# Kernel tuning notes

Hardware: AMD Instinct MI355X
Metric: run time of the kernel (lower is better)

Reference implementation:

```python
import jax, jax.numpy as jnp
import numpy as np

N = 100000      # total nodes across all graphs
E = 1600000     # total directed edges (pred -> node)
F = 128         # feat_size
H = 128         # hidden_size
M = 128         # message_size
G = 8           # number of graphs in batch
NP = N // G     # nodes per graph (num_nodes entries, all equal)
CRITIC_W = 0.5  # critic_agg_weight


def _lin_init(key, fan_in, fan_out):
    s = 1.0 / np.sqrt(fan_in)
    return jax.random.uniform(key, (fan_in, fan_out), jnp.float32, -s, s)


def setup_inputs() -> dict:
    key = jax.random.key(0)
    ks = jax.random.split(key, 20)
    inputs = jax.random.normal(ks[0], (N, F), jnp.float32)
    edge_src = jax.random.randint(ks[1], (E,), 0, N)
    edge_dst = jax.random.randint(ks[2], (E,), 0, N)
    actions = jax.random.randint(ks[3], (G,), 0, NP)
    return {
        'inputs': inputs,
        'W_in': _lin_init(ks[4], F, H), 'b_in': jnp.zeros((H,), jnp.float32),
        'W_msg': _lin_init(ks[5], H, M), 'b_msg': jnp.zeros((M,), jnp.float32),
        'W_upd': _lin_init(ks[6], M + H, H), 'b_upd': jnp.zeros((H,), jnp.float32),
        'W_a1': _lin_init(ks[7], H, 16), 'b_a1': jnp.zeros((16,), jnp.float32),
        'W_a2': _lin_init(ks[8], 16, 1), 'b_a2': jnp.zeros((1,), jnp.float32),
        'W_c1': _lin_init(ks[9], H, 16), 'b_c1': jnp.zeros((16,), jnp.float32),
        'W_c2': _lin_init(ks[10], 16, 1), 'b_c2': jnp.zeros((1,), jnp.float32),
        'edge_src': edge_src, 'edge_dst': edge_dst, 'actions': actions,
    }


def reference(inputs, W_in, b_in, W_msg, b_msg, W_upd, b_upd,
              W_a1, b_a1, W_a2, b_a2, W_c1, b_c1, W_c2, b_c2,
              edge_src, edge_dst, actions):
    # InputModel: Linear + ReLU  (send_input=True)
    node_states = jax.nn.relu(inputs @ W_in + b_in)          # [N, H]
    # MessageModel: Linear + ReLU
    messages = jax.nn.relu(node_states @ W_msg + b_msg)      # [N, M]
    # _aggregate_all: per-node sum over predecessor messages (segment-sum over edges)
    agg = jax.ops.segment_sum(messages[edge_src], edge_dst, num_segments=N)  # [N, M]
    # UpdateModel: Linear(M+H, H) + ReLU (no goal)
    updates = jax.nn.relu(jnp.concatenate([agg, node_states], axis=1) @ W_upd + b_upd)  # [N, H]
    # ActorModel: per-node logit
    logits_all = (jax.nn.relu(updates @ W_a1 + b_a1) @ W_a2 + b_a2).reshape(G, NP)
    # CriticModel: per-node score, per-graph weighted max/mean pooling
    crit_all = (jax.nn.relu(updates @ W_c1 + b_c1) @ W_c2 + b_c2).reshape(G, NP)
    v = (crit_all.max(axis=1) * CRITIC_W + crit_all.mean(axis=1) * (1.0 - CRITIC_W))[:, None]  # [G,1]
    # Categorical(logits) per graph: log_prob of given action + entropy
    logp = jax.nn.log_softmax(logits_all, axis=1)            # [G, NP]
    log_prob = jnp.take_along_axis(logp, actions[:, None], axis=1)  # [G,1]
    ent = -jnp.sum(jnp.exp(logp) * logp, axis=1, keepdims=True)     # [G,1]
    return updates, actions, log_prob, ent, v
```

## Files before the change

### kernel.cpp

```cpp
#include <hip/hip_runtime.h>
#include <math.h>

typedef unsigned short u16;
typedef unsigned int   u32;
typedef unsigned char  u8;
typedef __attribute__((ext_vector_type(8))) short short8v;
typedef __attribute__((ext_vector_type(4))) float f32x4;
typedef __attribute__((ext_vector_type(2))) float f32x2;

__device__ __forceinline__ u16 f2bf(float x) {
    u32 u = __float_as_uint(x);
    u += 0x7FFFu + ((u >> 16) & 1u);
    return (u16)(u >> 16);
}

#if __has_builtin(__builtin_amdgcn_cvt_pk_fp8_f32) && __has_builtin(__builtin_amdgcn_cvt_pk_f32_fp8)
#define HW_FP8 1
#endif

__device__ __forceinline__ u8 f2fp8(float v) {
#ifdef HW_FP8
    return (u8)(__builtin_amdgcn_cvt_pk_fp8_f32(v, v, 0, false) & 0xFF);
#else
    if (v < 0.015625f) return (u8)__float2int_rn(v * 512.0f);
    u32 b = __float_as_uint(fminf(v, 448.0f));
    b += 0x7FFFF + ((b >> 20) & 1);
    return (u8)((((b >> 23) - 120) << 3) | ((b >> 20) & 7));
#endif
}

__device__ __forceinline__ void fp8x4_acc(u32 w, float* acc) {
#ifdef HW_FP8
    const f32x2 lo = __builtin_amdgcn_cvt_pk_f32_fp8(w, false);
    const f32x2 hi = __builtin_amdgcn_cvt_pk_f32_fp8(w, true);
    acc[0] += lo[0]; acc[1] += lo[1]; acc[2] += hi[0]; acc[3] += hi[1];
#else
#pragma unroll
    for (int i = 0; i < 4; ++i) {
        const u32 b = (w >> (8 * i)) & 0xFF;
        const u32 e = (b >> 3) & 15, m = b & 7;
        acc[i] += e ? __uint_as_float(((e + 120) << 23) | (m << 20))
                    : (float)m * 0x1p-9f;
    }
#endif
}

#define NPB        256
#define NPB_SHIFT  8
#define EBUF_CAP   4608
#define MAX_BUK    512
#define BCS        16
#define BIN_CHUNK  4096

__global__ __launch_bounds__(256) void conv_kernel(
    const float* __restrict__ W_in, const float* __restrict__ W_msg,
    const float* __restrict__ W_upd,
    const float* __restrict__ Wa1, const float* __restrict__ Wc1,
    u16* __restrict__ Wt_in, u16* __restrict__ Wt_msg,
    u16* __restrict__ Wt_upd, u16* __restrict__ Wh,
    int* __restrict__ bcursor)
{
    const int idx = blockIdx.x * 256 + threadIdx.x;
    if (idx < 16384) {
        const int c = idx >> 7, k = idx & 127;
        Wt_in[c * 128 + k] = f2bf(W_in[k * 128 + c]);
    } else if (idx < 32768) {
        const int i = idx - 16384;
        const int c = i >> 7, k = i & 127;
        Wt_msg[c * 128 + k] = f2bf(W_msg[k * 128 + c]);
    } else if (idx < 65536) {
        const int i = idx - 32768;
        const int c = i >> 8, k = i & 255;
        Wt_upd[c * 256 + k] = f2bf(W_upd[k * 128 + c]);
    } else if (idx < 69632) {
        const int i = idx - 65536;
        const int col = i >> 7, k = i & 127;
        const float v = (col < 16) ? Wa1[k * 16 + col] : Wc1[k * 16 + (col - 16)];
        Wh[col * 128 + k] = f2bf(v);
    } else if (idx < 69632 + MAX_BUK * BCS) {
        bcursor[idx - 69632] = 0;
    }
}

__global__ __launch_bounds__(1024) void bin_gemm1_kernel(
    const int* __restrict__ src, const int* __restrict__ dst,
    int* __restrict__ bcursor, int* __restrict__ ebuf,
    int E, int nbuk, int binGrid, int g1Grid,
    const float* __restrict__ X, const u16* __restrict__ Wt_in,
    const float* __restrict__ b_in, u16* __restrict__ ns, int rows)
{
    __shared__ u16 smem[128 * 136];
    const int tid = threadIdx.x;

    const int mn   = min(binGrid, g1Grid);
    const int half = 2 * mn;
    int role, widx;
    if ((int)blockIdx.x < half) {
        role = (int)blockIdx.x & 1;
        widx = (int)blockIdx.x >> 1;
    } else {
        const int r = (int)blockIdx.x - half;
        role = (binGrid > g1Grid) ? 1 : 0;
        widx = mn + r;
    }

    if (role == 1) {
        int* lcount = (int*)smem;
        int* lbase  = lcount + MAX_BUK;
        const int e0 = widx * BIN_CHUNK;
        const int e1 = min(e0 + BIN_CHUNK, E);
        for (int b = tid; b < nbuk; b += 1024) lcount[b] = 0;
        __syncthreads();

        int pay[4];
        u32 brk[4];
#pragma unroll
        for (int k = 0; k < 4; ++k) {
            const int i = e0 + tid + k * 1024;
            int payv = 0; u32 brkv = 0xFFFFFFFFu;
            if (i < e1) {
                const int d = dst[i];
                const int b = d >> NPB_SHIFT;
                const int r = atomicAdd(&lcount[b], 1);
                payv = (src[i] << NPB_SHIFT) | (d & (NPB - 1));
                brkv = ((u32)b << 16) | (u32)r;
            }
            pay[k] = payv; brk[k] = brkv;
        }
        __syncthreads();

        for (int b = tid; b < nbuk; b += 1024) {
            const int c = lcount[b];
            lbase[b] = c ? atomicAdd(&bcursor[b * BCS], c) : 0;
        }
        __syncthreads();

#pragma unroll
        for (int k = 0; k < 4; ++k) {
            if (brk[k] != 0xFFFFFFFFu) {
                const int b = (int)(brk[k] >> 16);
                const int p = lbase[b] + (int)(brk[k] & 0xFFFFu);
                ebuf[b * EBUF_CAP + min(p, EBUF_CAP - 1)] = pay[k];
            }
        }
        return;
    }

    u16 (*WtL)[136] = (u16(*)[136])smem;
    for (int i = tid; i < 2048; i += 1024)
        *(uint4*)&WtL[i >> 4][(i & 15) * 8] = ((const uint4*)Wt_in)[i];

    const int lane = tid & 63, wave = tid >> 6;
    const int lrow = lane & 15, lk = lane >> 4;
    const int r0 = widx * 256 + wave * 16;
    const int arow = r0 + lrow;
    const bool rowok = arow < rows;

    short8v a[4];
#pragma unroll
    for (int ks = 0; ks < 4; ++ks) {
        const int k = ks * 32 + lk * 8;
        short8v av = {};
        if (rowok) {
            const float* pf = X + (size_t)arow * 128 + k;
            const float4 x0 = *(const float4*)pf;
            const float4 x1 = *(const float4*)(pf + 4);
            u16 t[8] = {f2bf(x0.x), f2bf(x0.y), f2bf(x0.z), f2bf(x0.w),
                        f2bf(x1.x), f2bf(x1.y), f2bf(x1.z), f2bf(x1.w)};
            av = *(short8v*)t;
        }
        a[ks] = av;
    }
    __syncthreads();

    f32x4 acc[8];
#pragma unroll
    for (int n = 0; n < 8; ++n) acc[n] = (f32x4){0.f, 0.f, 0.f, 0.f};
#pragma unroll
    for (int ks = 0; ks < 4; ++ks) {
#pragma unroll
        for (int n = 0; n < 8; ++n) {
            const short8v b = *(const short8v*)&WtL[n * 16 + lrow][ks * 32 + lk * 8];
            acc[n] = __builtin_amdgcn_mfma_f32_16x16x32_bf16(a[ks], b, acc[n], 0, 0, 0);
        }
    }
#pragma unroll
    for (int reg = 0; reg < 4; ++reg) {
        const int row = r0 + lk * 4 + reg;
        if (row >= rows) continue;
#pragma unroll
        for (int n = 0; n < 8; ++n) {
            const float v = fmaxf(acc[n][reg] + b_in[n * 16 + lrow], 0.f);
            ns[(size_t)row * 128 + n * 16 + lrow] = f2bf(v);
        }
    }
}

__global__ __launch_bounds__(256) void csr_gemm2_kernel(
    const int* __restrict__ ebuf, const int* __restrict__ bcursor,
    int* __restrict__ offs, int* __restrict__ csr, int N, int E, int nbuk,
    const u16* __restrict__ ns, const u16* __restrict__ Wt_msg,
    const float* __restrict__ b_msg, u8* __restrict__ msg8, int rows, int g2Grid)
{
    __shared__ u16 smem[128 * 136];
    const int tid = threadIdx.x;

    if ((int)blockIdx.x >= g2Grid) {
        int* ibuf = (int*)smem;
        int* red  = ibuf;
        int* ndeg = ibuf + 4;
        int* nofs = ibuf + 260;
        int* ws   = ibuf + 516;
        int* wp   = ibuf + 520;
        const int b = (int)blockIdx.x - g2Grid;

        int part = 0;
        for (int i = tid; i < b; i += 256) part += bcursor[i * BCS];
#pragma unroll
        for (int off = 32; off >= 1; off >>= 1) part += __shfl_xor(part, off);
        if ((tid & 63) == 0) red[tid >> 6] = part;
        __syncthreads();
        const int base = red[0] + red[1] + red[2] + red[3];

        const int cnt = min(bcursor[b * BCS], EBUF_CAP);
        const int* eb = ebuf + b * EBUF_CAP;

        ndeg[tid] = 0;
        __syncthreads();
        for (int j = tid; j < cnt; j += 256)
            atomicAdd(&ndeg[eb[j] & (NPB - 1)], 1);
        __syncthreads();

        const int lane = tid & 63, wid = tid >> 6;
        const int v = ndeg[tid];
        int x = v;
#pragma unroll
        for (int off = 1; off < 64; off <<= 1) {
            const int y = __shfl_up(x, off);
            if (lane >= off) x += y;
        }
        if (lane == 63) ws[wid] = x;
        __syncthreads();
        if (tid == 0) { int s = 0; for (int w = 0; w < 4; ++w) { wp[w] = s; s += ws[w]; } }
        __syncthreads();
        const int excl = x - v + wp[wid];
        nofs[tid] = excl;
        const int node = (b << NPB_SHIFT) + tid;
        if (node < N) offs[node] = base + excl;
        if (b == 0 && tid == 0) offs[N] = E;
        ndeg[tid] = 0;
        __syncthreads();

        for (int j = tid; j < cnt; j += 256) {
            const int e = eb[j];
            const int d = e & (NPB - 1);
            const int p = atomicAdd(&ndeg[d], 1);
            csr[base + nofs[d] + p] = e >> NPB_SHIFT;
        }
        return;
    }

    u16 (*WtL)[136] = (u16(*)[136])smem;
    for (int i = tid; i < 2048; i += 256)
        *(uint4*)&WtL[i >> 4][(i & 15) * 8] = ((const uint4*)Wt_msg)[i];

    const int lane = tid & 63, wave = tid >> 6;
    const int lrow = lane & 15, lk = lane >> 4;
    const int r0 = (int)blockIdx.x * 64 + wave * 16;
    const int arow = r0 + lrow;
    const bool rowok = arow < rows;

    short8v a[4];
#pragma unroll
    for (int ks = 0; ks < 4; ++ks) {
        short8v av = {};
        if (rowok) av = *(const short8v*)(ns + (size_t)arow * 128 + ks * 32 + lk * 8);
        a[ks] = av;
    }
    __syncthreads();

    f32x4 acc[8];
#pragma unroll
    for (int n = 0; n < 8; ++n) acc[n] = (f32x4){0.f, 0.f, 0.f, 0.f};
#pragma unroll
    for (int ks = 0; ks < 4; ++ks) {
#pragma unroll
        for (int n = 0; n < 8; ++n) {
            const short8v b = *(const short8v*)&WtL[n * 16 + lrow][ks * 32 + lk * 8];
            acc[n] = __builtin_amdgcn_mfma_f32_16x16x32_bf16(a[ks], b, acc[n], 0, 0, 0);
        }
    }
#pragma unroll
    for (int reg = 0; reg < 4; ++reg) {
        const int row = r0 + lk * 4 + reg;
        if (row >= rows) continue;
#pragma unroll
        for (int n = 0; n < 8; ++n) {
            const float v = fmaxf(acc[n][reg] + b_msg[n * 16 + lrow], 0.f);
            msg8[(size_t)row * 128 + n * 16 + lrow] = f2fp8(v);
        }
    }
}

__device__ __forceinline__ void acc16(float* acc, const uint4 u) {
    fp8x4_acc(u.x, acc);
    fp8x4_acc(u.y, acc + 4);
    fp8x4_acc(u.z, acc + 8);
    fp8x4_acc(u.w, acc + 12);
}

__global__ __launch_bounds__(256) void gather_fp8_kernel(
    const int* __restrict__ offs, const int* __restrict__ csr,
    const u8* __restrict__ msg8, u16* __restrict__ agg, int N)
{
    const int node = blockIdx.x * 32 + (threadIdx.x >> 3);
    if (node >= N) return;
    const int c16 = threadIdx.x & 7;
    int j = offs[node];
    const int j1 = offs[node + 1];
    const uint4* mv = (const uint4*)msg8;
    float acc[16];
#pragma unroll
    for (int q = 0; q < 16; ++q) acc[q] = 0.f;
    for (; j + 3 < j1; j += 4) {
        const int s0 = csr[j], s1 = csr[j + 1], s2 = csr[j + 2], s3 = csr[j + 3];
        const uint4 u0 = mv[(size_t)s0 * 8 + c16];
        const uint4 u1 = mv[(size_t)s1 * 8 + c16];
        const uint4 u2 = mv[(size_t)s2 * 8 + c16];
        const uint4 u3 = mv[(size_t)s3 * 8 + c16];
        acc16(acc, u0); acc16(acc, u1); acc16(acc, u2); acc16(acc, u3);
    }
    for (; j < j1; ++j)
        acc16(acc, mv[(size_t)csr[j] * 8 + c16]);

    u16 r[16];
#pragma unroll
    for (int q = 0; q < 16; ++q) r[q] = f2bf(acc[q]);
    uint4* ap = (uint4*)(agg + (size_t)node * 128 + c16 * 16);
    ap[0] = *(uint4*)r;
    ap[1] = *(uint4*)(r + 8);
}

__global__ __launch_bounds__(512) void gemm3_head_kernel(
    const u16* __restrict__ agg, const u16* __restrict__ ns,
    const u16* __restrict__ Wt_upd, const float* __restrict__ b_upd,
    float* __restrict__ Cf,
    const u16* __restrict__ Wh,
    const float* __restrict__ ba1, const float* __restrict__ Wa2, const float* __restrict__ ba2,
    const float* __restrict__ bc1, const float* __restrict__ Wc2, const float* __restrict__ bc2,
    float* __restrict__ logits, float* __restrict__ crit, int rows)
{
    __shared__ u16 smem[128 * 136];
    u16 (*WtL)[136] = (u16(*)[136])smem;

    const int tid = threadIdx.x;
    const uint4* W4 = (const uint4*)Wt_upd;

    for (int i = tid; i < 2048; i += 512)
        *(uint4*)&WtL[i >> 4][(i & 15) * 8] = W4[(i >> 4) * 32 + (i & 15)];

    const int lane = tid & 63, wave = tid >> 6;
    const int lrow = lane & 15, lk = lane >> 4;
    const int r0 = blockIdx.x * 128 + wave * 16;
    const int arow = r0 + lrow;
    const bool rowok = arow < rows;

    short8v a[4], a2[4];
#pragma unroll
    for (int ks = 0; ks < 4; ++ks) {
        short8v av = {}, av2 = {};
        if (rowok) {
            av  = *(const short8v*)(agg + (size_t)arow * 128 + ks * 32 + lk * 8);
            av2 = *(const short8v*)(ns  + (size_t)arow * 128 + ks * 32 + lk * 8);
        }
        a[ks] = av; a2[ks] = av2;
    }
    __syncthreads();

    f32x4 acc[8];
#pragma unroll
    for (int n = 0; n < 8; ++n) acc[n] = (f32x4){0.f, 0.f, 0.f, 0.f};
#pragma unroll
    for (int ks = 0; ks < 4; ++ks) {
#pragma unroll
        for (int n = 0; n < 8; ++n) {
            const short8v b = *(const short8v*)&WtL[n * 16 + lrow][ks * 32 + lk * 8];
            acc[n] = __builtin_amdgcn_mfma_f32_16x16x32_bf16(a[ks], b, acc[n], 0, 0, 0);
        }
    }

    __syncthreads();
    for (int i = tid; i < 2048; i += 512)
        *(uint4*)&WtL[i >> 4][(i & 15) * 8] = W4[(i >> 4) * 32 + 16 + (i & 15)];
    __syncthreads();

#pragma unroll
    for (int ks = 0; ks < 4; ++ks) {
#pragma unroll
        for (int n = 0; n < 8; ++n) {
            const short8v b = *(const short8v*)&WtL[n * 16 + lrow][ks * 32 + lk * 8];
            acc[n] = __builtin_amdgcn_mfma_f32_16x16x32_bf16(a2[ks], b, acc[n], 0, 0, 0);
        }
    }

    u16 uv[4][8];
#pragma unroll
    for (int reg = 0; reg < 4; ++reg) {
        const int row = r0 + lk * 4 + reg;
#pragma unroll
        for (int n = 0; n < 8; ++n) {
            const float v = fmaxf(acc[n][reg] + b_upd[n * 16 + lrow], 0.f);
            uv[reg][n] = f2bf(v);
            if (row < rows) Cf[(size_t)row * 128 + n * 16 + lrow] = v;
        }
    }
    __syncthreads();

    u16 (*uT)[16][136] = (u16(*)[16][136])smem;
#pragma unroll
    for (int reg = 0; reg < 4; ++reg) {
        const int lr = lk * 4 + reg;
#pragma unroll
        for (int n = 0; n < 8; ++n)
            uT[wave][lr][n * 16 + lrow] = uv[reg][n];
    }
    __syncthreads();

    short8v ah[4], b0[4], b1[4];
#pragma unroll
    for (int ks = 0; ks < 4; ++ks) {
        const int k = ks * 32 + lk * 8;
        ah[ks] = *(const short8v*)&uT[wave][lrow][k];
        b0[ks] = *(const short8v*)(Wh + (size_t)lrow * 128 + k);
        b1[ks] = *(const short8v*)(Wh + (size_t)(16 + lrow) * 128 + k);
    }
    f32x4 acc0 = (f32x4){0.f, 0.f, 0.f, 0.f};
    f32x4 acc1 = (f32x4){0.f, 0.f, 0.f, 0.f};
#pragma unroll
    for (int ks = 0; ks < 4; ++ks) {
        acc0 = __builtin_amdgcn_mfma_f32_16x16x32_bf16(ah[ks], b0[ks], acc0, 0, 0, 0);
        acc1 = __builtin_amdgcn_mfma_f32_16x16x32_bf16(ah[ks], b1[ks], acc1, 0, 0, 0);
    }
    const float wa = Wa2[lrow], wc = Wc2[lrow];
    const float ha = ba1[lrow], hc = bc1[lrow];
    const float b2a = ba2[0],   b2c = bc2[0];
#pragma unroll
    for (int reg = 0; reg < 4; ++reg) {
        float pa = fmaxf(acc0[reg] + ha, 0.f) * wa;
        float pc = fmaxf(acc1[reg] + hc, 0.f) * wc;
#pragma unroll
        for (int off = 8; off >= 1; off >>= 1) {
            pa += __shfl_xor(pa, off);
            pc += __shfl_xor(pc, off);
        }
        const int row = r0 + lk * 4 + reg;
        if (lrow == 0 && row < rows) {
            logits[row] = pa + b2a;
            crit[row]   = pc + b2c;
        }
    }
}

__device__ __forceinline__ float blockRedMax(float v, float* red) {
#pragma unroll
    for (int o = 32; o >= 1; o >>= 1) v = fmaxf(v, __shfl_xor(v, o));
    const int w = threadIdx.x >> 6;
    __syncthreads();
    if ((threadIdx.x & 63) == 0) red[w] = v;
    __syncthreads();
    if (threadIdx.x < 16) {
        float x = red[threadIdx.x];
#pragma unroll
        for (int o = 8; o >= 1; o >>= 1) x = fmaxf(x, __shfl_xor(x, o));
        if (threadIdx.x == 0) red[0] = x;
    }
    __syncthreads();
    const float r = red[0];
    __syncthreads();
    return r;
}

__device__ __forceinline__ float blockRedSum(float v, float* red) {
#pragma unroll
    for (int o = 32; o >= 1; o >>= 1) v += __shfl_xor(v, o);
    const int w = threadIdx.x >> 6;
    __syncthreads();
    if ((threadIdx.x & 63) == 0) red[w] = v;
    __syncthreads();
    if (threadIdx.x < 16) {
        float x = red[threadIdx.x];
#pragma unroll
        for (int o = 8; o >= 1; o >>= 1) x += __shfl_xor(x, o);
        if (threadIdx.x == 0) red[0] = x;
    }
    __syncthreads();
    const float r = red[0];
    __syncthreads();
    return r;
}

__global__ __launch_bounds__(1024) void finalize_kernel(
    const float* __restrict__ logits, const float* __restrict__ crit,
    const int* __restrict__ actions, float* __restrict__ out, int NP, int G)
{
    __shared__ float slog[12512];
    __shared__ float red[16];
    const int g = blockIdx.x;
    const int tid = threadIdx.x;
    const float* lg = logits + (long long)g * NP;
    const float* cg = crit   + (long long)g * NP;

    float lmax = -3.402823466e38f, cmax = -3.402823466e38f, csum = 0.f;
    for (int i = tid; i < NP; i += 1024) {
        const float l = lg[i], c = cg[i];
        slog[i] = l;
        lmax = fmaxf(lmax, l);
        cmax = fmaxf(cmax, c);
        csum += c;
    }
    __syncthreads();
    lmax = blockRedMax(lmax, red);
    cmax = blockRedMax(cmax, red);
    csum = blockRedSum(csum, red);

    float zsum = 0.f, ssum = 0.f;
    for (int i = tid; i < NP; i += 1024) {
        const float s = slog[i];
        const float e = expf(s - lmax);
        zsum += e;
        ssum += s * e;
    }
    zsum = blockRedSum(zsum, red);
    ssum = blockRedSum(ssum, red);

    if (tid == 0) {
        const int a = actions[g];
        const float sa   = slog[a];
        const float logZ = logf(zsum) + lmax;
        const float lp   = sa - logZ;
        const float H    = logZ - ssum / zsum;
        const float v    = cmax * 0.5f + (csum / (float)NP) * 0.5f;
        out[g]         = (float)a;
        out[G + g]     = lp;
        out[2 * G + g] = H;
        out[3 * G + g] = v;
    }
}

extern "C" void kernel_launch(void* const* d_in, const int* in_sizes, int n_in,
                              void* d_out, int out_size, void* d_ws, size_t ws_size,
                              hipStream_t stream)
{
    const float* inputs = (const float*)d_in[0];
    const float* W_in   = (const float*)d_in[1];
    const float* b_in   = (const float*)d_in[2];
    const float* W_msg  = (const float*)d_in[3];
    const float* b_msg  = (const float*)d_in[4];
    const float* W_upd  = (const float*)d_in[5];
    const float* b_upd  = (const float*)d_in[6];
    const float* W_a1   = (const float*)d_in[7];
    const float* b_a1   = (const float*)d_in[8];
    const float* W_a2   = (const float*)d_in[9];
    const float* b_a2   = (const float*)d_in[10];
    const float* W_c1   = (const float*)d_in[11];
    const float* b_c1   = (const float*)d_in[12];
    const float* W_c2   = (const float*)d_in[13];
    const float* b_c2   = (const float*)d_in[14];
    const int* edge_src = (const int*)d_in[15];
    const int* edge_dst = (const int*)d_in[16];
    const int* actions  = (const int*)d_in[17];

    const int N  = in_sizes[0] / 128;
    const int E  = in_sizes[15];
    const int G  = in_sizes[17];
    const int NP = N / G;
    const int nbuk = (N + NPB - 1) >> NPB_SHIFT;

    float* out = (float*)d_out;

    u16* ns_bf  = (u16*)d_ws;
    u16* agg_bf = ns_bf + (size_t)N * 128;
    u8*  msg8   = (u8*)(agg_bf + (size_t)N * 128);
    u16* Wt_in  = (u16*)(msg8 + (size_t)N * 128);
    u16* Wt_msg = Wt_in  + 128 * 128;
    u16* Wt_upd = Wt_msg + 128 * 128;
    u16* Wh     = Wt_upd + 128 * 256;
    float* logits = (float*)(Wh + 32 * 128);
    float* crit   = logits + N;
    int*   offs    = (int*)(crit + N);
    int*   csr     = offs + (N + 1);
    int*   bcursor = csr + E;
    int*   ebuf    = bcursor + MAX_BUK * BCS;

    const int binGrid = (E + BIN_CHUNK - 1) / BIN_CHUNK;
    const int convGrid = (69632 + MAX_BUK * BCS + 255) / 256;
    const int g1Grid  = (N + 255) / 256;
    const int g2Grid  = (N + 63) / 64;
    const int g3Grid  = (N + 127) / 128;

    conv_kernel<<<convGrid, 256, 0, stream>>>(
        W_in, W_msg, W_upd, W_a1, W_c1, Wt_in, Wt_msg, Wt_upd, Wh, bcursor);
    bin_gemm1_kernel<<<binGrid + g1Grid, 1024, 0, stream>>>(
        edge_src, edge_dst, bcursor, ebuf, E, nbuk, binGrid, g1Grid,
        inputs, Wt_in, b_in, ns_bf, N);
    csr_gemm2_kernel<<<g2Grid + nbuk, 256, 0, stream>>>(
        ebuf, bcursor, offs, csr, N, E, nbuk,
        ns_bf, Wt_msg, b_msg, msg8, N, g2Grid);
    gather_fp8_kernel<<<(N + 31) / 32, 256, 0, stream>>>(offs, csr, msg8, agg_bf, N);
    gemm3_head_kernel<<<g3Grid, 512, 0, stream>>>(
        agg_bf, ns_bf, Wt_upd, b_upd, out, Wh,
        b_a1, W_a2, b_a2, b_c1, W_c2, b_c2, logits, crit, N);
    finalize_kernel<<<G, 1024, 0, stream>>>(logits, crit, actions, out + (size_t)N * 128, NP, G);
}
```

Before: 145.6 us.

## Split gather and update GEMM into halves and co-schedule them in one launch

Gather and update-GEMM work is split into two row halves. The first half is gathered alone. A combined kernel then runs the GEMM+head on the first half while other blocks gather the second half, and a final launch does the GEMM for the second half. The goal is to overlap the latency-bound gather with the compute-bound MFMA GEMM and reduce tail idle time. The cost is an extra kernel launch, and gather blocks now use 512 threads while sharing a kernel with the large static LDS allocation, which could reduce occupancy.

```diff
diff --git a/kernel.cpp b/kernel.cpp
--- a/kernel.cpp
+++ b/kernel.cpp
@@ -309,13 +309,14 @@
     fp8x4_acc(u.w, acc + 12);
 }
 
-__global__ __launch_bounds__(256) void gather_fp8_kernel(
+__device__ __forceinline__ void gather_body(
+    int tid, int widx, int rowBeg, int rowEnd,
     const int* __restrict__ offs, const int* __restrict__ csr,
-    const u8* __restrict__ msg8, u16* __restrict__ agg, int N)
-{
-    const int node = blockIdx.x * 32 + (threadIdx.x >> 3);
-    if (node >= N) return;
-    const int c16 = threadIdx.x & 7;
+    const u8* __restrict__ msg8, u16* __restrict__ agg)
+{
+    const int node = rowBeg + widx * 64 + (tid >> 3);
+    if (node >= rowEnd) return;
+    const int c16 = tid & 7;
     int j = offs[node];
     const int j1 = offs[node + 1];
     const uint4* mv = (const uint4*)msg8;
@@ -341,19 +342,16 @@
     ap[1] = *(uint4*)(r + 8);
 }
 
-__global__ __launch_bounds__(512) void gemm3_head_kernel(
+__device__ __forceinline__ void gemm3_head_body(
+    u16* smem_raw, int tid, int widx, int rowBeg, int rowEnd,
     const u16* __restrict__ agg, const u16* __restrict__ ns,
     const u16* __restrict__ Wt_upd, const float* __restrict__ b_upd,
-    float* __restrict__ Cf,
-    const u16* __restrict__ Wh,
+    float* __restrict__ Cf, const u16* __restrict__ Wh,
     const float* __restrict__ ba1, const float* __restrict__ Wa2, const float* __restrict__ ba2,
     const float* __restrict__ bc1, const float* __restrict__ Wc2, const float* __restrict__ bc2,
-    float* __restrict__ logits, float* __restrict__ crit, int rows)
-{
-    __shared__ u16 smem[128 * 136];
-    u16 (*WtL)[136] = (u16(*)[136])smem;
-
-    const int tid = threadIdx.x;
+    float* __restrict__ logits, float* __restrict__ crit)
+{
+    u16 (*WtL)[136] = (u16(*)[136])smem_raw;
     const uint4* W4 = (const uint4*)Wt_upd;
 
     for (int i = tid; i < 2048; i += 512)
@@ -361,9 +359,9 @@
 
     const int lane = tid & 63, wave = tid >> 6;
     const int lrow = lane & 15, lk = lane >> 4;
-    const int r0 = blockIdx.x * 128 + wave * 16;
+    const int r0 = rowBeg + widx * 128 + wave * 16;
     const int arow = r0 + lrow;
-    const bool rowok = arow < rows;
+    const bool rowok = arow < rowEnd;
 
     short8v a[4], a2[4];
 #pragma unroll
@@ -411,12 +409,12 @@
         for (int n = 0; n < 8; ++n) {
             const float v = fmaxf(acc[n][reg] + b_upd[n * 16 + lrow], 0.f);
             uv[reg][n] = f2bf(v);
-            if (row < rows) Cf[(size_t)row * 128 + n * 16 + lrow] = v;
-        }
-    }
-    __syncthreads();
-
-    u16 (*uT)[16][136] = (u16(*)[16][136])smem;
+            if (row < rowEnd) Cf[(size_t)row * 128 + n * 16 + lrow] = v;
+        }
+    }
+    __syncthreads();
+
+    u16 (*uT)[16][136] = (u16(*)[16][136])smem_raw;
 #pragma unroll
     for (int reg = 0; reg < 4; ++reg) {
         const int lr = lk * 4 + reg;
@@ -454,11 +452,55 @@
             pc += __shfl_xor(pc, off);
         }
         const int row = r0 + lk * 4 + reg;
-        if (lrow == 0 && row < rows) {
+        if (lrow == 0 && row < rowEnd) {
             logits[row] = pa + b2a;
             crit[row]   = pc + b2c;
         }
     }
+}
+
+__global__ __launch_bounds__(512) void gather_kernel(
+    const int* __restrict__ offs, const int* __restrict__ csr,
+    const u8* __restrict__ msg8, u16* __restrict__ agg, int rowBeg, int rowEnd)
+{
+    gather_body(threadIdx.x, blockIdx.x, rowBeg, rowEnd, offs, csr, msg8, agg);
+}
+
+__global__ __launch_bounds__(512) void gather_gemm3_kernel(
+    const int* __restrict__ offs, const int* __restrict__ csr,
+    const u8* __restrict__ msg8, u16* __restrict__ agg,
+    int gRowBeg, int gRowEnd,
+    const u16* __restrict__ ns,
+    const u16* __restrict__ Wt_upd, const float* __restrict__ b_upd,
+    float* __restrict__ Cf, const u16* __restrict__ Wh,
+    const float* __restrict__ ba1, const float* __restrict__ Wa2, const float* __restrict__ ba2,
+    const float* __restrict__ bc1, const float* __restrict__ Wc2, const float* __restrict__ bc2,
+    float* __restrict__ logits, float* __restrict__ crit,
+    int eRowBeg, int eRowEnd, int eBlocks)
+{
+    __shared__ u16 smem[128 * 136];
+    const int tid = threadIdx.x;
+    if ((int)blockIdx.x < eBlocks) {
+        gemm3_head_body(smem, tid, blockIdx.x, eRowBeg, eRowEnd,
+                        agg, ns, Wt_upd, b_upd, Cf, Wh,
+                        ba1, Wa2, ba2, bc1, Wc2, bc2, logits, crit);
+    } else {
+        gather_body(tid, (int)blockIdx.x - eBlocks, gRowBeg, gRowEnd, offs, csr, msg8, agg);
+    }
+}
+
+__global__ __launch_bounds__(512) void gemm3_head_kernel(
+    const u16* __restrict__ agg, const u16* __restrict__ ns,
+    const u16* __restrict__ Wt_upd, const float* __restrict__ b_upd,
+    float* __restrict__ Cf, const u16* __restrict__ Wh,
+    const float* __restrict__ ba1, const float* __restrict__ Wa2, const float* __restrict__ ba2,
+    const float* __restrict__ bc1, const float* __restrict__ Wc2, const float* __restrict__ bc2,
+    float* __restrict__ logits, float* __restrict__ crit, int rowBeg, int rowEnd)
+{
+    __shared__ u16 smem[128 * 136];
+    gemm3_head_body(smem, threadIdx.x, blockIdx.x, rowBeg, rowEnd,
+                    agg, ns, Wt_upd, b_upd, Cf, Wh,
+                    ba1, Wa2, ba2, bc1, Wc2, bc2, logits, crit);
 }
 
 __device__ __forceinline__ float blockRedMax(float v, float* red) {
@@ -596,7 +638,12 @@
     const int convGrid = (69632 + MAX_BUK * BCS + 255) / 256;
     const int g1Grid  = (N + 255) / 256;
     const int g2Grid  = (N + 63) / 64;
-    const int g3Grid  = (N + 127) / 128;
+
+    const int Nh = ((N / 2) + 127) & ~127;
+    const int gGridH0 = (Nh + 63) / 64;
+    const int gGridH1 = (N - Nh + 63) / 64;
+    const int eGridH0 = Nh / 128;
+    const int eGridH1 = (N - Nh + 127) / 128;
 
     conv_kernel<<<convGrid, 256, 0, stream>>>(
         W_in, W_msg, W_upd, W_a1, W_c1, Wt_in, Wt_msg, Wt_upd, Wh, bcursor);
@@ -606,9 +653,14 @@
     csr_gemm2_kernel<<<g2Grid + nbuk, 256, 0, stream>>>(
         ebuf, bcursor, offs, csr, N, E, nbuk,
         ns_bf, Wt_msg, b_msg, msg8, N, g2Grid);
-    gather_fp8_kernel<<<(N + 31) / 32, 256, 0, stream>>>(offs, csr, msg8, agg_bf, N);
-    gemm3_head_kernel<<<g3Grid, 512, 0, stream>>>(
+    gather_kernel<<<gGridH0, 512, 0, stream>>>(offs, csr, msg8, agg_bf, 0, Nh);
+    gather_gemm3_kernel<<<eGridH0 + gGridH1, 512, 0, stream>>>(
+        offs, csr, msg8, agg_bf, Nh, N,
+        ns_bf, Wt_upd, b_upd, out, Wh,
+        b_a1, W_a2, b_a2, b_c1, W_c2, b_c2, logits, crit,
+        0, Nh, eGridH0);
+    gemm3_head_kernel<<<eGridH1, 512, 0, stream>>>(
         agg_bf, ns_bf, Wt_upd, b_upd, out, Wh,
-        b_a1, W_a2, b_a2, b_c1, W_c2, b_c2, logits, crit, N);
+        b_a1, W_a2, b_a2, b_c1, W_c2, b_c2, logits, crit, Nh, N);
     finalize_kernel<<<G, 1024, 0, stream>>>(logits, crit, actions, out + (size_t)N * 128, NP, G);
 }
```

Result: slower. 170.3 us (+17.0%).
